# Kernel tuning notes

Hardware: AMD Instinct MI355X
Metric: run time of the kernel (lower is better)

The kernel has to match this reference:

```python
import jax, jax.numpy as jnp
import numpy as np
import math

MUL = 128
N_NODES = 10000
N_EDGES = 131072
AVG_NEIGH = 16.0
# (l1 of node irrep, l2 of edge SH, output l3); sorted by output irrep like e3nn Irreps.sort
INSTR = [(0, 0, 0), (1, 1, 0), (0, 1, 1), (1, 0, 1), (1, 2, 1), (0, 2, 2), (1, 1, 2), (1, 3, 2), (0, 3, 3), (1, 2, 3)]
SH_OFF = [0, 1, 4, 9]  # offsets of l-blocks inside edge_attrs (dim 16 = 1+3+5+7)


def _su2_cg(j1, j2, j3):
    f = math.factorial
    C = np.zeros((2 * j1 + 1, 2 * j2 + 1, 2 * j3 + 1))
    for m1 in range(-j1, j1 + 1):
        for m2 in range(-j2, j2 + 1):
            m3 = m1 + m2
            if abs(m3) > j3:
                continue
            pref = (2 * j3 + 1) * f(j3 + j1 - j2) * f(j3 - j1 + j2) * f(j1 + j2 - j3) / f(j1 + j2 + j3 + 1)
            pref *= f(j3 + m3) * f(j3 - m3) * f(j1 - m1) * f(j1 + m1) * f(j2 - m2) * f(j2 + m2)
            s = 0.0
            for k in range(max(0, -(j3 - j2 + m1), -(j3 - j1 - m2)), min(j1 + j2 - j3, j1 - m1, j2 + m2) + 1):
                s += (-1.0) ** k / (f(k) * f(j1 + j2 - j3 - k) * f(j1 - m1 - k) * f(j2 + m2 - k) * f(j3 - j2 + m1 + k) * f(j3 - j1 - m2 + k))
            C[m1 + j1, m2 + j2, m3 + j3] = math.sqrt(pref) * s
    return C


def _q(l):
    # change of basis real->complex spherical harmonics (e3nn convention incl. (-i)^l phase)
    q = np.zeros((2 * l + 1, 2 * l + 1), dtype=np.complex128)
    for m in range(-l, 0):
        q[l + m, l + abs(m)] = 1 / math.sqrt(2)
        q[l + m, l - abs(m)] = -1j / math.sqrt(2)
    q[l, l] = 1.0
    for m in range(1, l + 1):
        q[l + m, l + abs(m)] = (-1) ** m / math.sqrt(2)
        q[l + m, l - abs(m)] = 1j * (-1) ** m / math.sqrt(2)
    return ((-1j) ** l) * q


def _w3j(l1, l2, l3):
    C = _su2_cg(l1, l2, l3).astype(np.complex128)
    Q1, Q2, Q3 = _q(l1), _q(l2), _q(l3)
    for q3 in (np.conj(Q3), Q3):
        D = np.einsum('abc,ai,bj,ck->ijk', C, Q1, Q2, q3)
        if np.abs(D.imag).max() < 1e-9:
            Dr = D.real
            return (Dr / np.linalg.norm(Dr)).astype(np.float32)
    raise ValueError('real wigner-3j construction failed')


W3J = {ins: _w3j(ins[0], ins[1], ins[2]) for ins in set(INSTR)}


def setup_inputs():
    ks = jax.random.split(jax.random.key(0), 15)
    return {
        'node_feats': jax.random.normal(ks[0], (N_NODES, 4 * MUL), jnp.float32),
        'node_attrs': jax.random.normal(ks[1], (N_NODES, 10), jnp.float32),
        'edge_attrs': jax.random.normal(ks[2], (N_EDGES, 16), jnp.float32),
        'edge_feats': jax.random.normal(ks[3], (N_EDGES, 8), jnp.float32),
        'edge_index': jax.random.randint(ks[4], (2, N_EDGES), 0, N_NODES, jnp.int32),
        'W_node_0': jax.random.normal(ks[5], (MUL, MUL), jnp.float32),
        'W_node_1': jax.random.normal(ks[6], (MUL, MUL), jnp.float32),
        'R_W0': jax.random.normal(ks[7], (8, 64), jnp.float32),
        'R_W1': jax.random.normal(ks[8], (64, 64), jnp.float32),
        'R_W2': jax.random.normal(ks[9], (64, 64), jnp.float32),
        'R_W3': jax.random.normal(ks[10], (64, len(INSTR) * MUL), jnp.float32),
        'W_out_0': jax.random.normal(ks[11], (2 * MUL, MUL), jnp.float32),
        'W_out_1': jax.random.normal(ks[12], (3 * MUL, MUL), jnp.float32),
        'W_out_2': jax.random.normal(ks[13], (3 * MUL, MUL), jnp.float32),
        'W_out_3': jax.random.normal(ks[14], (2 * MUL, MUL), jnp.float32),
    }


def reference(node_feats, node_attrs, edge_attrs, edge_feats, edge_index, W_node_0, W_node_1, R_W0, R_W1, R_W2, R_W3, W_out_0, W_out_1, W_out_2, W_out_3):
    sender, receiver = edge_index[0], edge_index[1]
    n = node_feats.shape[0]
    # self-interaction Linear (e3nn: per-irrep matmul, weight / sqrt(fan_in))
    h0 = jnp.einsum('nui,uv->nvi', node_feats[:, :MUL].reshape(n, MUL, 1), W_node_0) / math.sqrt(MUL)
    h1 = jnp.einsum('nui,uv->nvi', node_feats[:, MUL:].reshape(n, MUL, 3), W_node_1) / math.sqrt(MUL)
    # radial MLP [8,64,64,64,1280] with SiLU on hidden layers
    r = edge_feats
    for W in (R_W0, R_W1, R_W2):
        r = jax.nn.silu(r @ (W / math.sqrt(W.shape[0])))
    r = r @ (R_W3 / math.sqrt(R_W3.shape[0]))
    hs = (h0[sender], h1[sender])  # gather sender feats, [E, MUL, 2l1+1]
    outs = {0: [], 1: [], 2: [], 3: []}
    for k, (l1, l2, l3) in enumerate(INSTR):
        w3j = jnp.asarray(W3J[(l1, l2, l3)])
        sh = edge_attrs[:, SH_OFF[l2]:SH_OFF[l2] + 2 * l2 + 1]
        w = r[:, k * MUL:(k + 1) * MUL]
        hw = hs[l1] * w[:, :, None]                                    # radial-weighted sender feats
        c = jnp.einsum('ijk,ej->eik', w3j, sh)                         # [E, 2l1+1, 2l3+1]
        t = jnp.einsum('eik,eui->euk', c, hw) * math.sqrt(2 * l3 + 1)  # 'uvu' path, component-norm path weight
        outs[l3].append(jax.ops.segment_sum(t, receiver, num_segments=n))
    Wout = (W_out_0, W_out_1, W_out_2, W_out_3)
    blocks = []
    for l in range(4):
        cat = jnp.concatenate(outs[l], axis=1)  # simplify(): concat multiplicities per l
        blocks.append(jnp.einsum('nui,uv->nvi', cat, Wout[l]) / (math.sqrt(cat.shape[1]) * AVG_NEIGH))
    return jnp.concatenate(blocks, axis=-1)  # reshape_irreps -> [N, MUL, 16]
```

## Files before the change

kernel.cpp:

```cpp
#include <hip/hip_runtime.h>
#include <math.h>

#define NNODES 10000
#define NEDGES 131072

#define W3J_OFF 0
#define H_OFF   1280
#define R2_OFF  (H_OFF + NNODES*512)
#define CC_OFF  (R2_OFF + NEDGES*64)
#define CNT_W   (CC_OFF + NEDGES*88)
#define CUR_W   (CNT_W + NNODES)
#define OFF_W   (CUR_W + NNODES)
#define ELIST_W (OFF_W + NNODES + 1)
#define SP_W    (ELIST_W + NEDGES)
#define WP_W    (((SP_W + NEDGES) + 3) & ~3)

constexpr int cL1[10]  = {0,1,0,1,1,0,1,1,0,1};
constexpr int cL2[10]  = {0,1,1,0,2,2,1,3,3,2};
constexpr int cN3[10]  = {1,1,3,3,3,5,5,5,7,7};
constexpr int cSHO[10] = {0,1,1,0,4,4,1,9,9,4};
constexpr int cCCO[11] = {0,1,4,7,16,25,30,45,60,67,88};
constexpr int cCATO[10]= {0,128,256,640,1024,1408,2048,2688,3328,4224};

struct cpx { double re, im; };
__device__ inline cpx cmul(cpx a, cpx b){ return {a.re*b.re - a.im*b.im, a.re*b.im + a.im*b.re}; }

__device__ double dfact(int n){ double r = 1.0; for (int i = 2; i <= n; ++i) r *= (double)i; return r; }

__device__ double cgval(int j1,int j2,int j3,int m1,int m2){
  int m3 = m1 + m2;
  if (m3 > j3 || m3 < -j3) return 0.0;
  double pref = (double)(2*j3+1) * dfact(j3+j1-j2)*dfact(j3-j1+j2)*dfact(j1+j2-j3)/dfact(j1+j2+j3+1);
  pref *= dfact(j3+m3)*dfact(j3-m3)*dfact(j1-m1)*dfact(j1+m1)*dfact(j2-m2)*dfact(j2+m2);
  int k0 = 0; if (-(j3-j2+m1) > k0) k0 = -(j3-j2+m1); if (-(j3-j1-m2) > k0) k0 = -(j3-j1-m2);
  int k1 = j1+j2-j3; if (j1-m1 < k1) k1 = j1-m1; if (j2+m2 < k1) k1 = j2+m2;
  double s = 0.0;
  for (int k = k0; k <= k1; ++k){
    double d = dfact(k)*dfact(j1+j2-j3-k)*dfact(j1-m1-k)*dfact(j2+m2-k)*dfact(j3-j2+m1+k)*dfact(j3-j1-m2+k);
    s += ((k & 1) ? -1.0 : 1.0) / d;
  }
  return sqrt(pref) * s;
}

__device__ cpx qval(int l, int a, int col){
  int m = a - l;
  const double is2 = 0.70710678118654752440;
  double re = 0.0, im = 0.0;
  if (m < 0){
    if (col == l - m) re = is2;
    else if (col == l + m) im = -is2;
  } else if (m == 0){
    if (col == l) re = 1.0;
  } else {
    double sgn = (m & 1) ? -1.0 : 1.0;
    if (col == l + m) re = sgn * is2;
    else if (col == l - m) im = sgn * is2;
  }
  double pr, pi;
  switch (l & 3){ case 0: pr=1; pi=0; break; case 1: pr=0; pi=-1; break; case 2: pr=-1; pi=0; break; default: pr=0; pi=1; }
  return { re*pr - im*pi, re*pi + im*pr };
}

__global__ void w3j_kernel(float* ws){
  __shared__ double red[128];
  __shared__ int useConjS;
  __shared__ double normS;
  const int IL[10][3] = {{0,0,0},{1,1,0},{0,1,1},{1,0,1},{1,2,1},{0,2,2},{1,1,2},{1,3,2},{0,3,3},{1,2,3}};
  int k = blockIdx.x;
  int l1 = IL[k][0], l2 = IL[k][1], l3 = IL[k][2];
  int n1 = 2*l1+1, n2 = 2*l2+1, n3 = 2*l3+1;
  int nent = n1*n2*n3;
  int tid = threadIdx.x;
  double dcr=0, dci=0, dpr=0, dpi=0;
  if (tid < nent){
    int i = tid/(n2*n3), j = (tid/n3)%n2, kk = tid%n3;
    for (int a = 0; a < n1; ++a){
      for (int b = 0; b < n2; ++b){
        int m1 = a - l1, m2 = b - l2, m3 = m1 + m2;
        if (m3 < -l3 || m3 > l3) continue;
        int c = m3 + l3;
        double C = cgval(l1,l2,l3,m1,m2);
        if (C == 0.0) continue;
        cpx q1 = qval(l1,a,i), q2 = qval(l2,b,j), q3 = qval(l3,c,kk);
        cpx t = cmul(q1,q2);
        cpx q3c = { q3.re, -q3.im };
        cpx tc = cmul(t, q3c);
        cpx tp = cmul(t, q3);
        dcr += C*tc.re; dci += C*tc.im;
        dpr += C*tp.re; dpi += C*tp.im;
      }
    }
  }
  red[tid] = (tid < nent) ? fabs(dci) : 0.0;
  __syncthreads();
  if (tid == 0){
    double mx = 0.0;
    for (int t = 0; t < 128; ++t) if (red[t] > mx) mx = red[t];
    useConjS = (mx < 1e-9) ? 1 : 0;
  }
  __syncthreads();
  double re = useConjS ? dcr : dpr;
  red[tid] = (tid < nent) ? re*re : 0.0;
  __syncthreads();
  if (tid == 0){
    double s = 0.0;
    for (int t = 0; t < 128; ++t) s += red[t];
    normS = sqrt(s);
  }
  __syncthreads();
  if (tid < nent)
    ws[W3J_OFF + k*128 + tid] = (float)(re / normS * sqrt((double)(2*l3+1)));
}

__launch_bounds__(256, 4)
__global__ void node_kernel(const float* __restrict__ nf, const float* __restrict__ W0,
                            const float* __restrict__ W1, float* __restrict__ ws){
  __shared__ float AtL[128*68];
  float* h = ws + H_OFF;
  int tid = threadIdx.x;
  int n0 = blockIdx.x * 64;
  const float rs = 0.08838834764831845f;
  int mg = (tid & 15) * 4;
  int vg = (tid >> 4) * 8;
  for (int c = 0; c < 4; ++c){
    __syncthreads();
    for (int idx = tid; idx < 8192; idx += 256){
      int m = idx >> 7, u = idx & 127;
      int node = n0 + m;
      float v = 0.f;
      if (node < NNODES)
        v = (c == 0) ? nf[(size_t)node*512 + u] : nf[(size_t)node*512 + 128 + u*3 + (c-1)];
      AtL[u*68 + m] = v;
    }
    __syncthreads();
    const float* W = (c == 0) ? W0 : W1;
    float acc[8][4];
    #pragma unroll
    for (int a = 0; a < 8; ++a){ acc[a][0]=0.f; acc[a][1]=0.f; acc[a][2]=0.f; acc[a][3]=0.f; }
    for (int u = 0; u < 128; ++u){
      float4 am = *(const float4*)&AtL[u*68 + mg];
      const float* wr = W + u*128 + vg;
      float4 b0 = *(const float4*)wr;
      float4 b1 = *(const float4*)(wr + 4);
      float aa[4] = {am.x, am.y, am.z, am.w};
      float bb[8] = {b0.x,b0.y,b0.z,b0.w,b1.x,b1.y,b1.z,b1.w};
      #pragma unroll
      for (int a = 0; a < 8; ++a)
        #pragma unroll
        for (int e = 0; e < 4; ++e)
          acc[a][e] += bb[a]*aa[e];
    }
    #pragma unroll
    for (int e = 0; e < 4; ++e){
      int node = n0 + mg + e;
      if (node < NNODES){
        float4 s0 = {acc[0][e]*rs, acc[1][e]*rs, acc[2][e]*rs, acc[3][e]*rs};
        float4 s1 = {acc[4][e]*rs, acc[5][e]*rs, acc[6][e]*rs, acc[7][e]*rs};
        *(float4*)&h[(size_t)node*512 + c*128 + vg] = s0;
        *(float4*)&h[(size_t)node*512 + c*128 + vg + 4] = s1;
      }
    }
  }
}

template<int KDIM>
__device__ __forceinline__ void mlp_layer(const float* __restrict__ Wg, const float* aL,
                                          float* oL, int tid, float scale){
  int eg = (tid & 15) * 4;
  int jg = (tid >> 4) * 4;
  float acc[4][4];
  #pragma unroll
  for (int a = 0; a < 4; ++a){ acc[a][0]=0.f; acc[a][1]=0.f; acc[a][2]=0.f; acc[a][3]=0.f; }
  #pragma unroll 4
  for (int i = 0; i < KDIM; ++i){
    float4 a4 = *(const float4*)&aL[i*68 + eg];
    float4 b4 = *(const float4*)&Wg[i*64 + jg];
    float aa[4] = {a4.x,a4.y,a4.z,a4.w};
    float bb[4] = {b4.x,b4.y,b4.z,b4.w};
    #pragma unroll
    for (int a = 0; a < 4; ++a)
      #pragma unroll
      for (int e = 0; e < 4; ++e)
        acc[a][e] += bb[a]*aa[e];
  }
  #pragma unroll
  for (int a = 0; a < 4; ++a){
    float4 st;
    float x0 = acc[a][0]*scale; st.x = x0/(1.f + expf(-x0));
    float x1 = acc[a][1]*scale; st.y = x1/(1.f + expf(-x1));
    float x2 = acc[a][2]*scale; st.z = x2/(1.f + expf(-x2));
    float x3 = acc[a][3]*scale; st.w = x3/(1.f + expf(-x3));
    *(float4*)&oL[(jg+a)*68 + eg] = st;
  }
}

__launch_bounds__(256)
__global__ void r2_kernel(const float* __restrict__ ef,
                          const float* __restrict__ RW0, const float* __restrict__ RW1,
                          const float* __restrict__ RW2, float* __restrict__ wsf){
  __shared__ float bufA[64*68];
  __shared__ float bufB[64*68];
  __shared__ float r2T[64*68];
  float* R2 = wsf + R2_OFF;
  int tid = threadIdx.x;
  int eb = blockIdx.x * 64;
  float* efT = r2T;
  for (int idx = tid; idx < 512; idx += 256){
    int e = idx >> 3, i2 = idx & 7;
    efT[i2*68 + e] = ef[(size_t)(eb+e)*8 + i2];
  }
  __syncthreads();
  mlp_layer<8 >(RW0, efT, bufA, tid, 0.35355339059327373f);
  __syncthreads();
  mlp_layer<64>(RW1, bufA, bufB, tid, 0.125f);
  __syncthreads();
  mlp_layer<64>(RW2, bufB, r2T, tid, 0.125f);
  __syncthreads();
  for (int idx = tid; idx < 4096; idx += 256){
    int e = idx >> 6, i = idx & 63;
    R2[((size_t)(eb+e) << 6) + i] = r2T[i*68 + e];
  }
}

__global__ void hist_kernel(const int* __restrict__ ei, int* __restrict__ cnt){
  int e = blockIdx.x*256 + threadIdx.x;
  if (e < NEDGES) atomicAdd(&cnt[ei[NEDGES + e]], 1);
}

__global__ void scan_kernel(const int* __restrict__ cnt, int* __restrict__ off){
  __shared__ int part[256];
  __shared__ int partp[256];
  int t = threadIdx.x;
  const int S = 40;
  int s = 0;
  for (int j = 0; j < S; ++j){ int idx = t*S + j; if (idx < NNODES) s += cnt[idx]; }
  part[t] = s;
  __syncthreads();
  if (t == 0){ int run = 0; for (int i = 0; i < 256; ++i){ partp[i] = run; run += part[i]; } }
  __syncthreads();
  int run = partp[t];
  for (int j = 0; j < S; ++j){
    int idx = t*S + j;
    if (idx <= NNODES){
      off[idx] = run;
      if (idx < NNODES) run += cnt[idx];
    }
  }
}

__global__ void fill_kernel(const int* __restrict__ ei, const int* __restrict__ off,
                            int* __restrict__ cur, int* __restrict__ elist){
  int e = blockIdx.x*256 + threadIdx.x;
  if (e < NEDGES){
    int r = ei[NEDGES + e];
    int p = off[r] + atomicAdd(&cur[r], 1);
    elist[p] = e;
  }
}

__launch_bounds__(256)
__global__ void sort_kernel(const int* __restrict__ ei, const int* __restrict__ off,
                            int* __restrict__ elist, int* __restrict__ sP){
  __shared__ int idsL[512];
  int n = blockIdx.x, tid = threadIdx.x;
  int beg = off[n], end = off[n+1];
  int deg = end - beg;
  int degc = deg < 512 ? deg : 512;
  for (int idx = tid; idx < degc; idx += 256) idsL[idx] = elist[beg + idx];
  __syncthreads();
  {
    int v0 = 0, r0 = 0, v1 = 0, r1 = 0;
    bool a0 = tid < degc, a1 = tid + 256 < degc;
    if (a0){ v0 = idsL[tid]; int r = 0; for (int j = 0; j < degc; ++j) r += (idsL[j] < v0); r0 = r; }
    if (a1){ v1 = idsL[tid+256]; int r = 0; for (int j = 0; j < degc; ++j) r += (idsL[j] < v1); r1 = r; }
    __syncthreads();
    if (a0) idsL[r0] = v0;
    if (a1) idsL[r1] = v1;
  }
  __syncthreads();
  for (int idx = tid; idx < degc; idx += 256){
    int id = idsL[idx];
    elist[beg + idx] = id;
    sP[beg + idx] = ei[id];
  }
  for (int idx = degc + tid; idx < deg; idx += 256)
    sP[beg + idx] = ei[elist[beg + idx]];
}

__device__ __forceinline__ float cc_compute(int r, const float* w3L, const float* she){
  float v = 0.f;
  #pragma unroll
  for (int in = 0; in < 10; ++in){
    if (r >= cCCO[in] && r < cCCO[in+1]){
      int rr = r - cCCO[in];
      const int N3v = cN3[in];
      const int N2v = 2*cL2[in] + 1;
      int i = rr / N3v;
      int q = rr - i*N3v;
      float s = 0.f;
      for (int j = 0; j < N2v; ++j)
        s += w3L[in*128 + (i*N2v + j)*N3v + q] * she[cSHO[in] + j];
      v = s;
    }
  }
  return v;
}

__launch_bounds__(256)
__global__ void cc_kernel(const float* __restrict__ ea, const int* __restrict__ elist,
                          float* __restrict__ wsf){
  __shared__ float w3L[1280];
  __shared__ float shE[32*16];
  __shared__ int eidL[32];
  float* ccP = wsf + CC_OFF;
  int tid = threadIdx.x;
  int pb = blockIdx.x * 32;
  for (int idx = tid; idx < 1280; idx += 256) w3L[idx] = wsf[W3J_OFF + idx];
  if (tid < 32) eidL[tid] = elist[pb + tid];
  __syncthreads();
  for (int idx = tid; idx < 512; idx += 256){
    int e = idx >> 4, j = idx & 15;
    shE[e*16 + j] = ea[((size_t)eidL[e] << 4) + j];
  }
  __syncthreads();
  for (int idx = tid; idx < 32*88; idx += 256){
    int e = idx / 88, r = idx - e*88;
    ccP[(size_t)pb*88 + (size_t)e*88 + r] = cc_compute(r, w3L, shE + e*16);
  }
}

__launch_bounds__(256)
__global__ void wk_kernel(const float* __restrict__ RW3, const float* __restrict__ wsf,
                          const int* __restrict__ elist, float* __restrict__ Wp,
                          int passBeg, int passCount){
  __shared__ float r2T[64*68];
  __shared__ int eidW[64];
  const float* R2 = wsf + R2_OFF;
  int tid = threadIdx.x;
  int p0 = passBeg + blockIdx.x * 64;
  int pEnd = passBeg + passCount;
  if (tid < 64){
    int p = p0 + tid;
    eidW[tid] = (p < pEnd) ? elist[p] : 0;
  }
  __syncthreads();
  for (int idx = tid; idx < 4096; idx += 256){
    int e = idx >> 6, i = idx & 63;
    float v = 0.f;
    if (p0 + e < pEnd) v = R2[((size_t)eidW[e] << 6) + i];
    r2T[i*68 + e] = v;
  }
  __syncthreads();
  int mg = (tid & 15) * 4;
  int vg = (tid >> 4) * 8;
  for (int nt = 0; nt < 10; ++nt){
    float acc[8][4];
    #pragma unroll
    for (int a = 0; a < 8; ++a){ acc[a][0]=0.f; acc[a][1]=0.f; acc[a][2]=0.f; acc[a][3]=0.f; }
    const float* wb = RW3 + nt*128 + vg;
    for (int i = 0; i < 64; ++i){
      float4 am = *(const float4*)&r2T[i*68 + mg];
      const float* wr = wb + (size_t)i*1280;
      float4 b0 = *(const float4*)wr;
      float4 b1 = *(const float4*)(wr + 4);
      float aa[4] = {am.x, am.y, am.z, am.w};
      float bb[8] = {b0.x,b0.y,b0.z,b0.w,b1.x,b1.y,b1.z,b1.w};
      #pragma unroll
      for (int a = 0; a < 8; ++a)
        #pragma unroll
        for (int e = 0; e < 4; ++e)
          acc[a][e] += bb[a]*aa[e];
    }
    #pragma unroll
    for (int e = 0; e < 4; ++e){
      int p = p0 + mg + e;
      if (p < pEnd){
        float* op = Wp + (size_t)(p - passBeg)*1280 + nt*128 + vg;
        float4 s0 = {acc[0][e]*0.125f, acc[1][e]*0.125f, acc[2][e]*0.125f, acc[3][e]*0.125f};
        float4 s1 = {acc[4][e]*0.125f, acc[5][e]*0.125f, acc[6][e]*0.125f, acc[7][e]*0.125f};
        *(float4*)op = s0;
        *(float4*)(op + 4) = s1;
      }
    }
  }
}

template<int IN, int NA>
__device__ __forceinline__ void tp_r(const float* __restrict__ cce, float4 hvv,
                                     float wvv, float (&accm)[NA]){
  constexpr int N3v = cN3[IN];
  const float* c = cce + cCCO[IN];
  if constexpr (cL1[IN] == 0){
    float wh = wvv * hvv.x;
    #pragma unroll
    for (int q = 0; q < N3v; ++q) accm[q] += c[q]*wh;
  } else {
    float wa = wvv*hvv.y, wb = wvv*hvv.z, wc = wvv*hvv.w;
    #pragma unroll
    for (int q = 0; q < N3v; ++q)
      accm[q] += c[q]*wa + c[N3v+q]*wb + c[2*N3v+q]*wc;
  }
}

template<int IN, int NA>
__device__ __forceinline__ void st_cat(float* catL, int u, const float (&accm)[NA]){
  constexpr int N3v = cN3[IN];
  float* p = catL + cCATO[IN] + u*N3v;
  #pragma unroll
  for (int q = 0; q < N3v; ++q) p[q] = accm[q];
}

template<int L>
__device__ __forceinline__ void out_l(const float* catL, const float* __restrict__ Wo,
                                      float* __restrict__ outp, int n, int v){
  constexpr int NI = 2*L + 1;
  constexpr int UL = (L==0 || L==3) ? 256 : 384;
  constexpr int GOv = (L==0) ? 0 : (L==1) ? 256 : (L==2) ? 1408 : 3328;
  constexpr int OOv = (L==0) ? 0 : (L==1) ? 1 : (L==2) ? 4 : 9;
  const float scale = (L==0 || L==3) ? 0.00390625f : 0.0031894435433133252f;
  float o[NI];
  #pragma unroll
  for (int i = 0; i < NI; ++i) o[i] = 0.f;
  #pragma unroll 4
  for (int ul = 0; ul < UL; ++ul){
    float wv = Wo[(size_t)ul*128 + v];
    const float* a = catL + GOv + ul*NI;
    #pragma unroll
    for (int i = 0; i < NI; ++i) o[i] += a[i]*wv;
  }
  float* op = outp + (size_t)n*2048 + v*16 + OOv;
  #pragma unroll
  for (int i = 0; i < NI; ++i) op[i] = o[i]*scale;
}

__launch_bounds__(256)
__global__ void gather_kernel(const float* __restrict__ wsf, const float* __restrict__ Wp,
                              const float* __restrict__ Wo0, const float* __restrict__ Wo1,
                              const float* __restrict__ Wo2, const float* __restrict__ Wo3,
                              const int* __restrict__ off, const int* __restrict__ sP,
                              float* __restrict__ outp,
                              int pass, int posPerPass, int passBeg){
  __shared__ float smemF[5120];
  float* ccL  = smemF;
  float* catL = smemF;
  const float* h   = wsf + H_OFF;
  const float* ccP = wsf + CC_OFF;
  int nblk = blockIdx.x, tid = threadIdx.x;
  int beg = off[nblk], end = off[nblk+1];
  int deg = end - beg;
  int myPass = (deg == 0) ? 0 : (beg / posPerPass);
  if (myPass != pass) return;

  int u = tid & 127;
  int i0 = tid >> 7;
  float acc0[1] = {0.f};
  float acc1[3] = {0.f,0.f,0.f};
  float acc2[5] = {0.f,0.f,0.f,0.f,0.f};
  float acc3[5] = {0.f,0.f,0.f,0.f,0.f};
  float acc4[7] = {0.f,0.f,0.f,0.f,0.f,0.f,0.f};

  for (int base = 0; base < deg; base += 8){
    int eN = deg - base; if (eN > 8) eN = 8;
    __syncthreads();
    {
      size_t cbase = (size_t)(beg + base) * 88;
      size_t cmax  = (size_t)NEDGES * 88 - 1;
      for (int idx = tid; idx < 704; idx += 256){
        size_t a = cbase + idx; if (a > cmax) a = cmax;
        ccL[idx] = ccP[a];
      }
    }
    __syncthreads();
    #pragma unroll
    for (int e = 0; e < 8; ++e){
      bool live = (e < eN);
      if (base + e >= deg && e >= eN) {  }
      int pe = beg + base + (live ? e : 0);
      const float* wr = Wp + (size_t)(pe - passBeg)*1280 + (i0 << 7) + u;
      float w0 = wr[0];
      float w1 = wr[256];
      float w2 = wr[512];
      float w3 = wr[768];
      float w4 = wr[1024];
      if (!live){ w0 = 0.f; w1 = 0.f; w2 = 0.f; w3 = 0.f; w4 = 0.f; }
      int s = sP[pe];
      const float* hp = h + ((size_t)s << 9);
      float4 hvv = { hp[u], hp[128 + u], hp[256 + u], hp[384 + u] };
      const float* cce = ccL + e*88;
      if (i0 == 0){
        tp_r<0>(cce, hvv, w0, acc0);
        tp_r<2>(cce, hvv, w1, acc1);
        tp_r<4>(cce, hvv, w2, acc2);
        tp_r<6>(cce, hvv, w3, acc3);
        tp_r<8>(cce, hvv, w4, acc4);
      } else {
        tp_r<1>(cce, hvv, w0, acc0);
        tp_r<3>(cce, hvv, w1, acc1);
        tp_r<5>(cce, hvv, w2, acc2);
        tp_r<7>(cce, hvv, w3, acc3);
        tp_r<9>(cce, hvv, w4, acc4);
      }
    }
  }
  __syncthreads();
  if (i0 == 0){
    st_cat<0>(catL, u, acc0);
    st_cat<2>(catL, u, acc1);
    st_cat<4>(catL, u, acc2);
    st_cat<6>(catL, u, acc3);
    st_cat<8>(catL, u, acc4);
  } else {
    st_cat<1>(catL, u, acc0);
    st_cat<3>(catL, u, acc1);
    st_cat<5>(catL, u, acc2);
    st_cat<7>(catL, u, acc3);
    st_cat<9>(catL, u, acc4);
  }
  __syncthreads();
  if (i0 == 0){
    out_l<0>(catL, Wo0, outp, nblk, u);
    out_l<2>(catL, Wo2, outp, nblk, u);
  } else {
    out_l<1>(catL, Wo1, outp, nblk, u);
    out_l<3>(catL, Wo3, outp, nblk, u);
  }
}

extern "C" void kernel_launch(void* const* d_in, const int* in_sizes, int n_in,
                              void* d_out, int out_size, void* d_ws, size_t ws_size,
                              hipStream_t stream){
  const float* nf  = (const float*)d_in[0];
  const float* ea  = (const float*)d_in[2];
  const float* ef  = (const float*)d_in[3];
  const int*   ei  = (const int*)d_in[4];
  const float* W0  = (const float*)d_in[5];
  const float* W1  = (const float*)d_in[6];
  const float* RW0 = (const float*)d_in[7];
  const float* RW1 = (const float*)d_in[8];
  const float* RW2 = (const float*)d_in[9];
  const float* RW3 = (const float*)d_in[10];
  const float* Wo0 = (const float*)d_in[11];
  const float* Wo1 = (const float*)d_in[12];
  const float* Wo2 = (const float*)d_in[13];
  const float* Wo3 = (const float*)d_in[14];
  float* wsf  = (float*)d_ws;
  int*   wsi  = (int*)d_ws;
  float* outp = (float*)d_out;

  int P = 32;
  {
    const size_t fixedWords = (size_t)WP_W;
    const int cands[6] = {1, 2, 4, 8, 16, 32};
    for (int ci = 0; ci < 6; ++ci){
      size_t need = (fixedWords + ((size_t)(NEDGES / cands[ci]) + 512) * 1280) * 4;
      if (need <= ws_size){ P = cands[ci]; break; }
    }
  }
  int posPerPass = NEDGES / P;

  hipMemsetAsync(wsi + CNT_W, 0, 2*NNODES*sizeof(int), stream);
  w3j_kernel<<<10, 128, 0, stream>>>(wsf);
  node_kernel<<<157, 256, 0, stream>>>(nf, W0, W1, wsf);
  r2_kernel<<<2048, 256, 0, stream>>>(ef, RW0, RW1, RW2, wsf);
  hist_kernel<<<512, 256, 0, stream>>>(ei, wsi + CNT_W);
  scan_kernel<<<1, 256, 0, stream>>>(wsi + CNT_W, wsi + OFF_W);
  fill_kernel<<<512, 256, 0, stream>>>(ei, wsi + OFF_W, wsi + CUR_W, wsi + ELIST_W);
  sort_kernel<<<NNODES, 256, 0, stream>>>(ei, wsi + OFF_W, wsi + ELIST_W, wsi + SP_W);
  cc_kernel<<<NEDGES/32, 256, 0, stream>>>(ea, wsi + ELIST_W, wsf);

  for (int p = 0; p < P; ++p){
    int passBeg = p * posPerPass;
    int passCount = posPerPass + 512;
    if (passBeg + passCount > NEDGES) passCount = NEDGES - passBeg;
    int wkBlocks = (passCount + 63) / 64;
    wk_kernel<<<wkBlocks, 256, 0, stream>>>(RW3, wsf, wsi + ELIST_W, wsf + WP_W,
                                            passBeg, passCount);
    gather_kernel<<<NNODES, 256, 0, stream>>>(wsf, wsf + WP_W, Wo0, Wo1, Wo2, Wo3,
                                              wsi + OFF_W, wsi + SP_W, outp,
                                              p, posPerPass, passBeg);
  }
}
```

Before: 1.984 ms.

## Interleave node features and radial weights so gather uses vectorized float4 loads

Node features h are now stored interleaved with the component index fastest ([node][u][4]). The per-edge radial weights are split into a float4-interleaved buffer for the first four paths plus a separate buffer for the fifth. This lets the gather kernel fetch each thread's feature vector and four weights with single float4 loads instead of strided scalar loads. Sender indices are staged in shared memory, the cc tile copy is vectorized, and an output loop is unrolled further. The cost is uncoalesced strided scalar stores in the producer kernels.

```diff
diff --git a/kernel.cpp b/kernel.cpp
--- a/kernel.cpp
+++ b/kernel.cpp
@@ -154,10 +154,10 @@
     for (int e = 0; e < 4; ++e){
       int node = n0 + mg + e;
       if (node < NNODES){
-        float4 s0 = {acc[0][e]*rs, acc[1][e]*rs, acc[2][e]*rs, acc[3][e]*rs};
-        float4 s1 = {acc[4][e]*rs, acc[5][e]*rs, acc[6][e]*rs, acc[7][e]*rs};
-        *(float4*)&h[(size_t)node*512 + c*128 + vg] = s0;
-        *(float4*)&h[(size_t)node*512 + c*128 + vg + 4] = s1;
+        float* hb = h + (size_t)node*512 + c;
+        #pragma unroll
+        for (int a = 0; a < 8; ++a)
+          hb[(vg + a)*4] = acc[a][e]*rs;
       }
     }
   }
@@ -325,13 +325,14 @@
   __syncthreads();
   for (int idx = tid; idx < 32*88; idx += 256){
     int e = idx / 88, r = idx - e*88;
-    ccP[(size_t)pb*88 + (size_t)e*88 + r] = cc_compute(r, w3L, shE + e*16);
+    ccP[(size_t)(pb+e)*88 + r] = cc_compute(r, w3L, shE + e*16);
   }
 }
 
 __launch_bounds__(256)
 __global__ void wk_kernel(const float* __restrict__ RW3, const float* __restrict__ wsf,
-                          const int* __restrict__ elist, float* __restrict__ Wp,
+                          const int* __restrict__ elist,
+                          float* __restrict__ Wp4, float* __restrict__ Wp1,
                           int passBeg, int passCount){
   __shared__ float r2T[64*68];
   __shared__ int eidW[64];
@@ -371,15 +372,22 @@
         for (int e = 0; e < 4; ++e)
           acc[a][e] += bb[a]*aa[e];
     }
+    int m  = nt >> 1;
+    int tb = ((nt & 1) << 7) + vg;
     #pragma unroll
     for (int e = 0; e < 4; ++e){
       int p = p0 + mg + e;
       if (p < pEnd){
-        float* op = Wp + (size_t)(p - passBeg)*1280 + nt*128 + vg;
-        float4 s0 = {acc[0][e]*0.125f, acc[1][e]*0.125f, acc[2][e]*0.125f, acc[3][e]*0.125f};
-        float4 s1 = {acc[4][e]*0.125f, acc[5][e]*0.125f, acc[6][e]*0.125f, acc[7][e]*0.125f};
-        *(float4*)op = s0;
-        *(float4*)(op + 4) = s1;
+        size_t pw = (size_t)(p - passBeg);
+        if (nt < 8){
+          float* op = Wp4 + pw*1024 + (size_t)tb*4 + m;
+          #pragma unroll
+          for (int a = 0; a < 8; ++a) op[a*4] = acc[a][e]*0.125f;
+        } else {
+          float* op = Wp1 + pw*256 + tb;
+          #pragma unroll
+          for (int a = 0; a < 8; ++a) op[a] = acc[a][e]*0.125f;
+        }
       }
     }
   }
@@ -421,7 +429,7 @@
   float o[NI];
   #pragma unroll
   for (int i = 0; i < NI; ++i) o[i] = 0.f;
-  #pragma unroll 4
+  #pragma unroll 8
   for (int ul = 0; ul < UL; ++ul){
     float wv = Wo[(size_t)ul*128 + v];
     const float* a = catL + GOv + ul*NI;
@@ -434,13 +442,15 @@
 }
 
 __launch_bounds__(256)
-__global__ void gather_kernel(const float* __restrict__ wsf, const float* __restrict__ Wp,
+__global__ void gather_kernel(const float* __restrict__ wsf,
+                              const float* __restrict__ Wp4, const float* __restrict__ Wp1,
                               const float* __restrict__ Wo0, const float* __restrict__ Wo1,
                               const float* __restrict__ Wo2, const float* __restrict__ Wo3,
                               const int* __restrict__ off, const int* __restrict__ sP,
                               float* __restrict__ outp,
                               int pass, int posPerPass, int passBeg){
   __shared__ float smemF[5120];
+  __shared__ int   sCL[8];
   float* ccL  = smemF;
   float* catL = smemF;
   const float* h   = wsf + H_OFF;
@@ -463,42 +473,38 @@
     int eN = deg - base; if (eN > 8) eN = 8;
     __syncthreads();
     {
-      size_t cbase = (size_t)(beg + base) * 88;
-      size_t cmax  = (size_t)NEDGES * 88 - 1;
-      for (int idx = tid; idx < 704; idx += 256){
-        size_t a = cbase + idx; if (a > cmax) a = cmax;
-        ccL[idx] = ccP[a];
-      }
+      const float4* src = (const float4*)(ccP + (size_t)(beg + base)*88);
+      float4* dst = (float4*)ccL;
+      for (int idx = tid; idx < 176; idx += 256) dst[idx] = src[idx];
+    }
+    if (tid < 8){
+      int k = base + tid;
+      sCL[tid] = sP[beg + ((k < deg) ? k : base)];
     }
     __syncthreads();
     #pragma unroll
     for (int e = 0; e < 8; ++e){
       bool live = (e < eN);
-      if (base + e >= deg && e >= eN) {  }
       int pe = beg + base + (live ? e : 0);
-      const float* wr = Wp + (size_t)(pe - passBeg)*1280 + (i0 << 7) + u;
-      float w0 = wr[0];
-      float w1 = wr[256];
-      float w2 = wr[512];
-      float w3 = wr[768];
-      float w4 = wr[1024];
-      if (!live){ w0 = 0.f; w1 = 0.f; w2 = 0.f; w3 = 0.f; w4 = 0.f; }
-      int s = sP[pe];
-      const float* hp = h + ((size_t)s << 9);
-      float4 hvv = { hp[u], hp[128 + u], hp[256 + u], hp[384 + u] };
+      size_t pw = (size_t)(pe - passBeg);
+      float4 w4v = *(const float4*)&Wp4[pw*1024 + (tid << 2)];
+      float  w1v = Wp1[pw*256 + tid];
+      if (!live){ w4v.x = 0.f; w4v.y = 0.f; w4v.z = 0.f; w4v.w = 0.f; w1v = 0.f; }
+      int s = sCL[e];
+      float4 hvv = *(const float4*)&h[((size_t)s << 9) + (u << 2)];
       const float* cce = ccL + e*88;
       if (i0 == 0){
-        tp_r<0>(cce, hvv, w0, acc0);
-        tp_r<2>(cce, hvv, w1, acc1);
-        tp_r<4>(cce, hvv, w2, acc2);
-        tp_r<6>(cce, hvv, w3, acc3);
-        tp_r<8>(cce, hvv, w4, acc4);
+        tp_r<0>(cce, hvv, w4v.x, acc0);
+        tp_r<2>(cce, hvv, w4v.y, acc1);
+        tp_r<4>(cce, hvv, w4v.z, acc2);
+        tp_r<6>(cce, hvv, w4v.w, acc3);
+        tp_r<8>(cce, hvv, w1v,   acc4);
       } else {
-        tp_r<1>(cce, hvv, w0, acc0);
-        tp_r<3>(cce, hvv, w1, acc1);
-        tp_r<5>(cce, hvv, w2, acc2);
-        tp_r<7>(cce, hvv, w3, acc3);
-        tp_r<9>(cce, hvv, w4, acc4);
+        tp_r<1>(cce, hvv, w4v.x, acc0);
+        tp_r<3>(cce, hvv, w4v.y, acc1);
+        tp_r<5>(cce, hvv, w4v.z, acc2);
+        tp_r<7>(cce, hvv, w4v.w, acc3);
+        tp_r<9>(cce, hvv, w1v,   acc4);
       }
     }
   }
@@ -557,6 +563,9 @@
     }
   }
   int posPerPass = NEDGES / P;
+  size_t sliceEdges = (size_t)posPerPass + 512;
+  float* Wp4 = wsf + WP_W;
+  float* Wp1 = Wp4 + sliceEdges*1024;
 
   hipMemsetAsync(wsi + CNT_W, 0, 2*NNODES*sizeof(int), stream);
   w3j_kernel<<<10, 128, 0, stream>>>(wsf);
@@ -573,9 +582,9 @@
     int passCount = posPerPass + 512;
     if (passBeg + passCount > NEDGES) passCount = NEDGES - passBeg;
     int wkBlocks = (passCount + 63) / 64;
-    wk_kernel<<<wkBlocks, 256, 0, stream>>>(RW3, wsf, wsi + ELIST_W, wsf + WP_W,
+    wk_kernel<<<wkBlocks, 256, 0, stream>>>(RW3, wsf, wsi + ELIST_W, Wp4, Wp1,
                                             passBeg, passCount);
-    gather_kernel<<<NNODES, 256, 0, stream>>>(wsf, wsf + WP_W, Wo0, Wo1, Wo2, Wo3,
+    gather_kernel<<<NNODES, 256, 0, stream>>>(wsf, Wp4, Wp1, Wo0, Wo1, Wo2, Wo3,
                                               wsi + OFF_W, wsi + SP_W, outp,
                                               p, posPerPass, passBeg);
   }
```

New measurement: 2.248 ms. +13.3%, slower.
